# Optimization experiments

Measured on AMD Instinct MI355X. Metric: run time of the kernel, lower is better.

Reference implementation:

```python
import jax, jax.numpy as jnp
import numpy as np

H = 8        # num_heads
LN_EPS = 1e-5
NEG = -1000000.0


def setup_inputs() -> dict:
    key = jax.random.key(0)
    ks = jax.random.split(key, 8)
    B, T, D = 4, 4096, 1024
    s = 1.0 / np.sqrt(D)
    x = jax.random.normal(ks[0], (B, T, D), dtype=jnp.float32)
    tmask = (jnp.arange(T) < (3 * T) // 4).astype(jnp.float32)
    src_mask = jnp.broadcast_to(tmask[None, :, None], (B, T, 1)).astype(jnp.float32)
    Wq = jax.random.normal(ks[1], (D, D), dtype=jnp.float32) * s
    Wk = jax.random.normal(ks[2], (D, D), dtype=jnp.float32) * s
    Wv = jax.random.normal(ks[3], (D, D), dtype=jnp.float32) * s
    bq = jnp.zeros((D,), jnp.float32)
    bk = jnp.zeros((D,), jnp.float32)
    bv = jnp.zeros((D,), jnp.float32)
    gamma = jnp.ones((D,), jnp.float32)
    beta = jnp.zeros((D,), jnp.float32)
    return {"x": x, "src_mask": src_mask, "Wq": Wq, "bq": bq, "Wk": Wk,
            "bk": bk, "Wv": Wv, "bv": bv, "gamma": gamma, "beta": beta}


def reference(x, src_mask, Wq, bq, Wk, bk, Wv, bv, gamma, beta):
    B, T, D = x.shape
    Dh = D // H
    # LayerNorm (same normed input feeds q, k, v)
    mu = jnp.mean(x, axis=-1, keepdims=True)
    var = jnp.mean(jnp.square(x - mu), axis=-1, keepdims=True)
    xn = (x - mu) * jax.lax.rsqrt(var + LN_EPS) * gamma + beta
    q = xn @ Wq + bq                               # [B,T,D]
    k = xn @ Wk + bk + (1.0 - src_mask) * NEG      # mask padded timesteps
    v = (xn @ Wv + bv) * src_mask                  # zero padded values
    q = jax.nn.softmax(q.reshape(B, T, H, Dh), axis=-1)   # over feature dim
    k = jax.nn.softmax(k.reshape(B, T, H, Dh), axis=1)    # over time dim
    v = v.reshape(B, T, H, Dh)
    # efficient/linear attention: O(T * Dh^2) per head
    att = jnp.einsum('bnhd,bnhl->bhdl', k, v)      # [B,H,Dh,Dh]
    y = jnp.einsum('bnhd,bhdl->bnhl', q, att).reshape(B, T, D)
    return x + y
```

## Files before the change

kernel.cpp:

```cpp
#include <hip/hip_runtime.h>
#include <stdint.h>


typedef unsigned short u16;
typedef __attribute__((ext_vector_type(8))) short bf16x8;
typedef __attribute__((ext_vector_type(4))) float f32x4;

__device__ u16 g_WT[3][1024 * 1024];
__device__ u16 g_xn[16777216];
__device__ u16 g_ekT[16777216];
__device__ u16 g_vvT[16777216];
__device__ float g_attp[8388608];
__device__ u16 g_attT[524288];
__device__ float g_Z[4096];
__device__ int g_mflag[64];

__device__ __forceinline__ float b2f(u16 u) {
  union { unsigned int i; float f; } c;
  c.i = ((unsigned int)u) << 16;
  return c.f;
}
__device__ __forceinline__ u16 f2b(float f) {
  union { float f; unsigned int i; } c;
  c.f = f;
  unsigned int r = c.i + 0x7fffu + ((c.i >> 16) & 1u);
  return (u16)(r >> 16);
}

__device__ __forceinline__ void gload16(const void* g, void* l) {
  __builtin_amdgcn_global_load_lds(
      reinterpret_cast<const __attribute__((address_space(1))) uint32_t*>(
          reinterpret_cast<uintptr_t>(g)),
      reinterpret_cast<__attribute__((address_space(3))) uint32_t*>(
          reinterpret_cast<uintptr_t>(l)),
      16, 0, 0);
}

__device__ __forceinline__ void stage128x32(const u16* g, int stride, char* lds,
                                            int wave, int lane) {
  const int r = wave * 32 + (lane >> 2);
  const int cb = (lane & 3) * 16;
  const char* gp = (const char*)g;
  gload16(gp + (size_t)r * stride * 2 + cb, lds + wave * 2048);
  gload16(gp + (size_t)(r + 16) * stride * 2 + cb, lds + wave * 2048 + 1024);
}

__device__ __forceinline__ bf16x8 frag_ld(const char* lds, int row, int lane) {
  return *(const bf16x8*)(lds + row * 64 + ((lane >> 4) * 16));
}

__device__ __forceinline__ void tile_mfma(const char* As, const char* Bs,
                                          f32x4 (&acc)[4][4], int wm, int wn,
                                          int lane) {
  bf16x8 af[4], bfr[4];
#pragma unroll
  for (int i = 0; i < 4; i++) af[i] = frag_ld(As, wm * 64 + i * 16 + (lane & 15), lane);
#pragma unroll
  for (int j = 0; j < 4; j++) bfr[j] = frag_ld(Bs, wn * 64 + j * 16 + (lane & 15), lane);
#pragma unroll
  for (int i = 0; i < 4; i++)
#pragma unroll
    for (int j = 0; j < 4; j++)
      acc[i][j] = __builtin_amdgcn_mfma_f32_16x16x32_bf16(af[i], bfr[j], acc[i][j], 0, 0, 0);
}

__device__ __forceinline__ void stageA256(char* buf, const u16* gsrc, int h,
                                          int wave, int lane) {
#pragma unroll
  for (int i = 0; i < 2; i++) {
    const int ib = i * 64 + wave * 8;
    const int rowb = (ib & 63) | ((ib & 64) << 1) | (h << 6);
    const int row = rowb + (lane >> 3);
    const int cc = (lane & 7) ^ (row & 7);
    gload16((const char*)gsrc + ((size_t)row * 1024 + cc * 8) * 2,
            buf + rowb * 128);
  }
}
__device__ __forceinline__ void stageB256(char* buf, const u16* gsrc, int h,
                                          int wave, int lane) {
#pragma unroll
  for (int i = 0; i < 2; i++) {
    const int ib = i * 64 + wave * 8;
    const int rowb = (ib & 31) | ((ib & 96) << 1) | (h << 5);
    const int row = rowb + (lane >> 3);
    const int cc = (lane & 7) ^ (row & 7);
    gload16((const char*)gsrc + ((size_t)row * 1024 + cc * 8) * 2,
            buf + rowb * 128);
  }
}
__device__ __forceinline__ bf16x8 fragS(const char* buf, int R, int ks, int lane) {
  const int q = lane >> 4;
  return *(const bf16x8*)(buf + R * 128 + ((((ks << 2) + q) ^ (R & 7)) << 4));
}

template <bool ST>
__device__ __forceinline__ void tile_1ph(char* Ab, char* Bb, char* An, char* Bn,
                                         const u16* Agn, const u16* Bgn,
                                         f32x4 (&acc)[8][4], int wave, int lane,
                                         int wm, int wn) {
  if constexpr (ST) {
    stageA256(An, Agn, 0, wave, lane);
    stageA256(An, Agn, 1, wave, lane);
    stageB256(Bn, Bgn, 0, wave, lane);
    stageB256(Bn, Bgn, 1, wave, lane);
  }
  bf16x8 a[4][2], b[4][2];
#pragma unroll
  for (int cf = 0; cf < 4; cf++) {
    const int R = wn * 64 + cf * 16 + (lane & 15);
#pragma unroll
    for (int ks = 0; ks < 2; ks++) b[cf][ks] = fragS(Bb, R, ks, lane);
  }
#pragma unroll
  for (int rf = 0; rf < 4; rf++) {
    const int R = wm * 128 + rf * 16 + (lane & 15);
#pragma unroll
    for (int ks = 0; ks < 2; ks++) a[rf][ks] = fragS(Ab, R, ks, lane);
  }
  __builtin_amdgcn_s_setprio(1);
#pragma unroll
  for (int rf = 0; rf < 4; rf++)
#pragma unroll
    for (int cf = 0; cf < 4; cf++)
#pragma unroll
      for (int ks = 0; ks < 2; ks++)
        acc[rf][cf] = __builtin_amdgcn_mfma_f32_16x16x32_bf16(
            a[rf][ks], b[cf][ks], acc[rf][cf], 0, 0, 0);
  bf16x8 a2[4][2];
#pragma unroll
  for (int rf = 0; rf < 4; rf++) {
    const int R = wm * 128 + 64 + rf * 16 + (lane & 15);
#pragma unroll
    for (int ks = 0; ks < 2; ks++) a2[rf][ks] = fragS(Ab, R, ks, lane);
  }
#pragma unroll
  for (int rf = 0; rf < 4; rf++)
#pragma unroll
    for (int cf = 0; cf < 4; cf++)
#pragma unroll
      for (int ks = 0; ks < 2; ks++)
        acc[4 + rf][cf] = __builtin_amdgcn_mfma_f32_16x16x32_bf16(
            a2[rf][ks], b[cf][ks], acc[4 + rf][cf], 0, 0, 0);
  __builtin_amdgcn_s_setprio(0);
  if constexpr (ST) asm volatile("s_waitcnt vmcnt(0)" ::: "memory");
  __builtin_amdgcn_s_barrier();
  __builtin_amdgcn_sched_barrier(0);
}

__global__ __launch_bounds__(256) void prep_kernel(const float* __restrict__ x,
                                                   const float* __restrict__ gamma,
                                                   const float* __restrict__ beta,
                                                   const float* __restrict__ wq,
                                                   const float* __restrict__ wk,
                                                   const float* __restrict__ wv,
                                                   const float* __restrict__ mask) {
  __shared__ float ls[4], ls2[4];
  __shared__ u16 tile[32][33];
  __shared__ int sflag;
  const int bid = blockIdx.x;
  const int tid = threadIdx.x;
  if (bid < 16384) {
    if (bid < 16) g_Z[bid * 256 + tid] = 0.0f;
    if (bid < 64) {
      if (tid == 0) sflag = 0;
      __syncthreads();
      if (mask[bid * 256 + tid] > 0.5f) atomicOr(&sflag, 1);
      __syncthreads();
      if (tid == 0) g_mflag[bid] = sflag;
    }
    const int wave = tid >> 6, lane = tid & 63;
    const float* xr = x + (size_t)bid * 1024;
    float4 u = ((const float4*)xr)[tid];
    float v0 = u.x, v1 = u.y, v2 = u.z, v3 = u.w;
    float s = v0 + v1 + v2 + v3;
    float s2 = v0 * v0 + v1 * v1 + v2 * v2 + v3 * v3;
#pragma unroll
    for (int off = 32; off > 0; off >>= 1) {
      s += __shfl_down(s, off);
      s2 += __shfl_down(s2, off);
    }
    if (lane == 0) { ls[wave] = s; ls2[wave] = s2; }
    __syncthreads();
    s = ls[0] + ls[1] + ls[2] + ls[3];
    s2 = ls2[0] + ls2[1] + ls2[2] + ls2[3];
    const float mu = s * (1.0f / 1024.0f);
    const float var = fmaxf(s2 * (1.0f / 1024.0f) - mu * mu, 0.0f);
    const float rstd = rsqrtf(var + 1e-5f);
    float4 g4 = ((const float4*)gamma)[tid];
    float4 be = ((const float4*)beta)[tid];
    ushort4 o;
    o.x = f2b((v0 - mu) * rstd * g4.x + be.x);
    o.y = f2b((v1 - mu) * rstd * g4.y + be.y);
    o.z = f2b((v2 - mu) * rstd * g4.z + be.z);
    o.w = f2b((v3 - mu) * rstd * g4.w + be.w);
    *(ushort4*)(g_xn + (size_t)bid * 1024 + tid * 4) = o;
  } else {
    const int id = bid - 16384;
    const int which = id >> 10;
    const int rem = id & 1023;
    const float* src = (which == 0) ? wq : (which == 1) ? wk : wv;
    u16* dst = g_WT[which];
    const int tx = tid & 31;
    const int ty = tid >> 5;
    const int c0 = (rem & 31) * 32, r0 = (rem >> 5) * 32;
#pragma unroll
    for (int i = 0; i < 4; i++)
      tile[ty + i * 8][tx] = f2b(src[(size_t)(r0 + ty + i * 8) * 1024 + c0 + tx]);
    __syncthreads();
#pragma unroll
    for (int i = 0; i < 4; i++)
      dst[(size_t)(c0 + ty + i * 8) * 1024 + r0 + tx] = tile[tx][ty + i * 8];
  }
}

__global__ __launch_bounds__(512, 2) void gemm_kv(const float* __restrict__ bk,
                                                  const float* __restrict__ bv,
                                                  const float* __restrict__ mask) {
  __shared__ __align__(16) char smem[131072];
  const int tid = threadIdx.x, wave = tid >> 6, lane = tid & 63;
  const int L = blockIdx.x;
  const int mt = (L & 7) + 8 * (L >> 6);
  const int nt = (L >> 3) & 7;
  const int n0 = (nt & 3) * 256;
  const int z = nt >> 2;
  const int m0 = mt * 256;
  const u16* wt = z ? g_WT[2] : g_WT[1];
  const float* bias = z ? bv : bk;
  u16* outT = z ? g_vvT : g_ekT;
  const int b = m0 >> 12;
  const int t0 = m0 & 4095;
  const int wm = wave >> 2, wn = wave & 3;
  const u16* Ag = g_xn + (size_t)m0 * 1024;
  const u16* Bg = wt + (size_t)n0 * 1024;
  const size_t gbase = (size_t)b * (1024 * 4096) + (size_t)n0 * 4096 + t0;

  if (!g_mflag[m0 >> 8]) {
    const uint4 zz = {0u, 0u, 0u, 0u};
#pragma unroll
    for (int u = 0; u < 16; u++) {
      const int id = u * 512 + tid;
      const int feat = id >> 5, c = id & 31;
      *(uint4*)(outT + gbase + (size_t)feat * 4096 + c * 8) = zz;
    }
    return;
  }

  f32x4 zero = {0.f, 0.f, 0.f, 0.f};
  f32x4 acc[8][4];
#pragma unroll
  for (int i = 0; i < 8; i++)
#pragma unroll
    for (int j = 0; j < 4; j++) acc[i][j] = zero;

  stageA256(smem, Ag, 0, wave, lane);
  stageA256(smem, Ag, 1, wave, lane);
  stageB256(smem + 65536, Bg, 0, wave, lane);
  stageB256(smem + 65536, Bg, 1, wave, lane);
  asm volatile("s_waitcnt vmcnt(0)" ::: "memory");
  __builtin_amdgcn_s_barrier();

#pragma unroll 1
  for (int t = 0; t < 15; ++t) {
    const int p = t & 1;
    tile_1ph<true>(smem + p * 32768, smem + 65536 + p * 32768,
                   smem + (p ^ 1) * 32768, smem + 65536 + (p ^ 1) * 32768,
                   Ag + (t + 1) * 64, Bg + (t + 1) * 64, acc, wave, lane, wm, wn);
  }
  tile_1ph<false>(smem + 32768, smem + 65536 + 32768, smem, smem + 65536, Ag,
                  Bg, acc, wave, lane, wm, wn);

  u16* tT = (u16*)smem;
  float fsum[4] = {0.f, 0.f, 0.f, 0.f};
#pragma unroll
  for (int rf = 0; rf < 8; rf++)
#pragma unroll
    for (int r = 0; r < 4; r++) {
      const int tok = wm * 128 + rf * 16 + (lane >> 4) * 4 + r;
      const float mv = mask[m0 + tok];
#pragma unroll
      for (int cf = 0; cf < 4; cf++) {
        const int feat = wn * 64 + cf * 16 + (lane & 15);
        const float aV = acc[rf][cf][r] + bias[n0 + feat];
        float o;
        if (z)
          o = aV * mv;
        else
          o = (mv > 0.5f) ? __expf(fminf(aV, 30.0f)) : 0.0f;
        const u16 ob = f2b(o);
        tT[feat * 256 + ((((tok >> 3) ^ (feat & 7)) << 3) | (tok & 7))] = ob;
        if (!z) fsum[cf] += b2f(ob);
      }
    }
  if (!z) {
#pragma unroll
    for (int cf = 0; cf < 4; cf++) {
      float s = fsum[cf];
      s += __shfl_xor(s, 16);
      s += __shfl_xor(s, 32);
      if (lane < 16)
        atomicAdd(&g_Z[b * 1024 + n0 + wn * 64 + cf * 16 + lane], s);
    }
  }
  __syncthreads();
#pragma unroll
  for (int u = 0; u < 16; u++) {
    const int id = u * 512 + tid;
    const int feat = id >> 5, c = id & 31;
    uint4 val = *(const uint4*)&tT[feat * 256 + ((c ^ (feat & 7)) << 3)];
    *(uint4*)(outT + gbase + (size_t)feat * 4096 + c * 8) = val;
  }
}

__global__ __launch_bounds__(256) void gemm_att() {
  __shared__ __align__(16) char smem[32768];
  char* A0 = smem;
  char* B0 = smem + 8192;
  char* A1 = smem + 16384;
  char* B1 = smem + 24576;
  const int tid = threadIdx.x, wave = tid >> 6, lane = tid & 63;
  const int kc = blockIdx.x;
  const int bh = blockIdx.y;
  const int b = bh >> 3, h = bh & 7;
  if (!(g_mflag[b * 16 + kc * 2] | g_mflag[b * 16 + kc * 2 + 1])) return;
  const size_t base = (size_t)b * (1024 * 4096) + (size_t)(h * 128) * 4096;
  const int wm = wave & 1, wn = wave >> 1;
  const u16* Ag = g_ekT + base + kc * 512;
  const u16* Bg = g_vvT + base + kc * 512;

  f32x4 zero = {0.f, 0.f, 0.f, 0.f};
  f32x4 acc[4][4];
#pragma unroll
  for (int i = 0; i < 4; i++)
#pragma unroll
    for (int j = 0; j < 4; j++) acc[i][j] = zero;

  stage128x32(Ag, 4096, A0, wave, lane);
  stage128x32(Bg, 4096, B0, wave, lane);
  __syncthreads();
  for (int kt = 0; kt < 512; kt += 64) {
    stage128x32(Ag + kt + 32, 4096, A1, wave, lane);
    stage128x32(Bg + kt + 32, 4096, B1, wave, lane);
    tile_mfma(A0, B0, acc, wm, wn, lane);
    __syncthreads();
    if (kt + 64 < 512) {
      stage128x32(Ag + kt + 64, 4096, A0, wave, lane);
      stage128x32(Bg + kt + 64, 4096, B0, wave, lane);
    }
    tile_mfma(A1, B1, acc, wm, wn, lane);
    __syncthreads();
  }

  float* op = g_attp + ((size_t)(kc * 32 + bh)) * 16384;
#pragma unroll
  for (int i = 0; i < 4; i++)
#pragma unroll
    for (int r = 0; r < 4; r++) {
      const int row = wm * 64 + i * 16 + (lane >> 4) * 4 + r;
#pragma unroll
      for (int j = 0; j < 4; j++) {
        const int col = wn * 64 + j * 16 + (lane & 15);
        op[row * 128 + col] = acc[i][j][r];
      }
    }
}

__global__ __launch_bounds__(256) void attnorm_kernel() {
  const int bh = blockIdx.x;
  const int b = bh >> 3, h = bh & 7;
  const int tid = threadIdx.x;
  __shared__ float Zl[128];
  __shared__ int vfl[8];
  if (tid < 128) Zl[tid] = fmaxf(g_Z[b * 1024 + h * 128 + tid], 1e-30f);
  if (tid < 8) vfl[tid] = g_mflag[b * 16 + tid * 2] | g_mflag[b * 16 + tid * 2 + 1];
  __syncthreads();
  const int i0 = blockIdx.y * 2048;
  for (int i = i0 + tid; i < i0 + 2048; i += 256) {
    const int d = i >> 7, l = i & 127;
    float s = 0.f;
#pragma unroll
    for (int c = 0; c < 8; c++)
      if (vfl[c]) s += g_attp[((size_t)(c * 32 + bh)) * 16384 + i];
    g_attT[(size_t)bh * 16384 + l * 128 + d] = f2b(s / Zl[d]);
  }
}

__global__ __launch_bounds__(512, 2) void gemm_qy(const float* __restrict__ bq,
                                                  const float* __restrict__ x,
                                                  float* __restrict__ out) {
  __shared__ __align__(16) char smem[131072];
  __shared__ float zq4[4][256];
  const int tid = threadIdx.x, wave = tid >> 6, lane = tid & 63;
  const int L = blockIdx.x;
  const int g = L >> 3;
  const int mt = (L & 7) + 8 * (g >> 2);
  const int n0 = (g & 3) * 256;
  const int m0 = mt * 256;
  const int b = m0 >> 12;
  const int wm = wave >> 2, wn = wave & 3;
  const u16* Ag = g_xn + (size_t)m0 * 1024;
  const u16* Bg = g_WT[0] + (size_t)n0 * 1024;

  f32x4 zero = {0.f, 0.f, 0.f, 0.f};
  f32x4 acc[8][4];
#pragma unroll
  for (int i = 0; i < 8; i++)
#pragma unroll
    for (int j = 0; j < 4; j++) acc[i][j] = zero;

  stageA256(smem, Ag, 0, wave, lane);
  stageA256(smem, Ag, 1, wave, lane);
  stageB256(smem + 65536, Bg, 0, wave, lane);
  stageB256(smem + 65536, Bg, 1, wave, lane);
  asm volatile("s_waitcnt vmcnt(0)" ::: "memory");
  __builtin_amdgcn_s_barrier();

#pragma unroll 1
  for (int t = 0; t < 15; ++t) {
    const int p = t & 1;
    tile_1ph<true>(smem + p * 32768, smem + 65536 + p * 32768,
                   smem + (p ^ 1) * 32768, smem + 65536 + (p ^ 1) * 32768,
                   Ag + (t + 1) * 64, Bg + (t + 1) * 64, acc, wave, lane, wm, wn);
  }
  tile_1ph<false>(smem + 32768, smem + 65536 + 32768, smem, smem + 65536, Ag,
                  Bg, acc, wave, lane, wm, wn);

  const int hl = wn >> 1;
  const int bhh = b * 8 + (n0 >> 7) + hl;
  const u16* attb = g_attT + ((size_t)bhh << 14);
  bf16x8 bpre[4][4];
#pragma unroll
  for (int ks = 0; ks < 4; ks++)
#pragma unroll
    for (int cf = 0; cf < 4; cf++) {
      const int l = (wn & 1) * 64 + cf * 16 + (lane & 15);
      bpre[ks][cf] = *(const bf16x8*)(attb + l * 128 + ks * 32 + (lane >> 4) * 8);
    }

  u16* qs = (u16*)smem;
#pragma unroll
  for (int rf = 0; rf < 8; rf++)
#pragma unroll
    for (int r = 0; r < 4; r++) {
      const int tok = wm * 128 + rf * 16 + (lane >> 4) * 4 + r;
      float rs = 0.f;
#pragma unroll
      for (int cf = 0; cf < 4; cf++) {
        const int f = wn * 64 + cf * 16 + (lane & 15);
        const float e = __expf(fminf(acc[rf][cf][r] + bq[n0 + f], 30.0f));
        qs[tok * 256 + ((((f >> 3) ^ (tok & 31)) << 3) | (f & 7))] = f2b(e);
        rs += e;
      }
      rs += __shfl_xor(rs, 1);
      rs += __shfl_xor(rs, 2);
      rs += __shfl_xor(rs, 4);
      rs += __shfl_xor(rs, 8);
      if ((lane & 15) == 0) zq4[wn][tok] = rs;
    }
  __syncthreads();

  f32x4 acc2[8][4];
#pragma unroll
  for (int i = 0; i < 8; i++)
#pragma unroll
    for (int j = 0; j < 4; j++) acc2[i][j] = zero;

#pragma unroll
  for (int ks = 0; ks < 4; ks++) {
    bf16x8 af[8];
#pragma unroll
    for (int rf = 0; rf < 8; rf++) {
      const int tok = wm * 128 + rf * 16 + (lane & 15);
      af[rf] = *(const bf16x8*)&qs[tok * 256 +
          ((((hl << 4) + (ks << 2) + (lane >> 4)) ^ (tok & 31)) << 3)];
    }
#pragma unroll
    for (int rf = 0; rf < 8; rf++)
#pragma unroll
      for (int cf = 0; cf < 4; cf++)
        acc2[rf][cf] = __builtin_amdgcn_mfma_f32_16x16x32_bf16(
            af[rf], bpre[ks][cf], acc2[rf][cf], 0, 0, 0);
  }

#pragma unroll
  for (int rf = 0; rf < 8; rf++)
#pragma unroll
    for (int r = 0; r < 4; r++) {
      const int tok = wm * 128 + rf * 16 + (lane >> 4) * 4 + r;
      const float zq =
          fmaxf(zq4[hl * 2][tok] + zq4[hl * 2 + 1][tok], 1e-30f);
      const size_t n = (size_t)(m0 + tok);
#pragma unroll
      for (int cf = 0; cf < 4; cf++) {
        const int f = wn * 64 + cf * 16 + (lane & 15);
        const size_t idx = n * 1024 + n0 + f;
        out[idx] = x[idx] + acc2[rf][cf][r] / zq;
      }
    }
}

extern "C" void kernel_launch(void* const* d_in, const int* in_sizes, int n_in,
                              void* d_out, int out_size, void* d_ws, size_t ws_size,
                              hipStream_t stream) {
  const float* x = (const float*)d_in[0];
  const float* mask = (const float*)d_in[1];
  const float* Wq = (const float*)d_in[2];
  const float* bq = (const float*)d_in[3];
  const float* Wk = (const float*)d_in[4];
  const float* bk = (const float*)d_in[5];
  const float* Wv = (const float*)d_in[6];
  const float* bv = (const float*)d_in[7];
  const float* gamma = (const float*)d_in[8];
  const float* beta = (const float*)d_in[9];
  float* out = (float*)d_out;
  (void)d_ws; (void)ws_size;

  prep_kernel<<<dim3(16384 + 3072), 256, 0, stream>>>(x, gamma, beta, Wq, Wk, Wv, mask);
  gemm_kv<<<dim3(512), 512, 0, stream>>>(bk, bv, mask);
  gemm_att<<<dim3(8, 32), 256, 0, stream>>>();
  attnorm_kernel<<<dim3(32, 8), 256, 0, stream>>>();
  gemm_qy<<<dim3(256), 512, 0, stream>>>(bq, x, out);
}
```

Measured before the change: 339.7 us.

## Shrink gemm_kv tiles to 128x256 with K=32 stages for higher occupancy

The K/V projection GEMM moves from 256x256 output tiles with 64-wide K stages to 128x256 tiles with 32-wide K stages. This halves LDS use and accumulator registers so four blocks can share a CU, and doubles the grid to 1024 blocks. The mask flags become 128-token granular so all-padded tiles are skipped more precisely, and the downstream flag reads are updated to match. The cost is less data reuse per tile (more A/B traffic per FLOP) and twice as many barrier-synchronised K steps.

After: 350.9 us. +3.3%, slower.

```diff
diff --git a/kernel.cpp b/kernel.cpp
--- a/kernel.cpp
+++ b/kernel.cpp
@@ -13,7 +13,7 @@
 __device__ float g_attp[8388608];
 __device__ u16 g_attT[524288];
 __device__ float g_Z[4096];
-__device__ int g_mflag[64];
+__device__ int g_mflag[128];
 
 __device__ __forceinline__ float b2f(u16 u) {
   union { unsigned int i; float f; } c;
@@ -141,6 +141,57 @@
       for (int ks = 0; ks < 2; ks++)
         acc[4 + rf][cf] = __builtin_amdgcn_mfma_f32_16x16x32_bf16(
             a2[rf][ks], b[cf][ks], acc[4 + rf][cf], 0, 0, 0);
+  __builtin_amdgcn_s_setprio(0);
+  if constexpr (ST) asm volatile("s_waitcnt vmcnt(0)" ::: "memory");
+  __builtin_amdgcn_s_barrier();
+  __builtin_amdgcn_sched_barrier(0);
+}
+
+__device__ __forceinline__ void stageA128(char* buf, const u16* gsrc,
+                                          int wave, int lane) {
+  const int row = wave * 16 + (lane >> 2);
+  const int cc = (lane & 3) ^ ((row >> 1) & 3);
+  gload16((const char*)gsrc + ((size_t)row * 1024 + cc * 8) * 2,
+          buf + wave * 1024);
+}
+__device__ __forceinline__ void stageB256x32(char* buf, const u16* gsrc,
+                                             int wave, int lane) {
+#pragma unroll
+  for (int i = 0; i < 2; i++) {
+    const int row = i * 128 + wave * 16 + (lane >> 2);
+    const int cc = (lane & 3) ^ ((row >> 1) & 3);
+    gload16((const char*)gsrc + ((size_t)row * 1024 + cc * 8) * 2,
+            buf + i * 8192 + wave * 1024);
+  }
+}
+__device__ __forceinline__ bf16x8 fragS32(const char* buf, int R, int lane) {
+  const int q = lane >> 4;
+  return *(const bf16x8*)(buf + R * 64 + (((q ^ ((R >> 1) & 3))) << 4));
+}
+
+template <bool ST>
+__device__ __forceinline__ void tile32(char* Ab, char* Bb, char* An, char* Bn,
+                                       const u16* Agn, const u16* Bgn,
+                                       f32x4 (&acc)[4][4], int wave, int lane,
+                                       int wm, int wn) {
+  if constexpr (ST) {
+    stageA128(An, Agn, wave, lane);
+    stageB256x32(Bn, Bgn, wave, lane);
+  }
+  bf16x8 a[4], b[4];
+#pragma unroll
+  for (int cf = 0; cf < 4; cf++)
+    b[cf] = fragS32(Bb, wn * 64 + cf * 16 + (lane & 15), lane);
+#pragma unroll
+  for (int rf = 0; rf < 4; rf++)
+    a[rf] = fragS32(Ab, wm * 64 + rf * 16 + (lane & 15), lane);
+  __builtin_amdgcn_s_setprio(1);
+#pragma unroll
+  for (int rf = 0; rf < 4; rf++)
+#pragma unroll
+    for (int cf = 0; cf < 4; cf++)
+      acc[rf][cf] = __builtin_amdgcn_mfma_f32_16x16x32_bf16(
+          a[rf], b[cf], acc[rf][cf], 0, 0, 0);
   __builtin_amdgcn_s_setprio(0);
   if constexpr (ST) asm volatile("s_waitcnt vmcnt(0)" ::: "memory");
   __builtin_amdgcn_s_barrier();
@@ -161,10 +212,10 @@
   const int tid = threadIdx.x;
   if (bid < 16384) {
     if (bid < 16) g_Z[bid * 256 + tid] = 0.0f;
-    if (bid < 64) {
+    if (bid < 128) {
       if (tid == 0) sflag = 0;
       __syncthreads();
-      if (mask[bid * 256 + tid] > 0.5f) atomicOr(&sflag, 1);
+      if (tid < 128 && mask[bid * 128 + tid] > 0.5f) atomicOr(&sflag, 1);
       __syncthreads();
       if (tid == 0) g_mflag[bid] = sflag;
     }
@@ -213,17 +264,18 @@
   }
 }
 
-__global__ __launch_bounds__(512, 2) void gemm_kv(const float* __restrict__ bk,
+__global__ __launch_bounds__(512, 4) void gemm_kv(const float* __restrict__ bk,
                                                   const float* __restrict__ bv,
                                                   const float* __restrict__ mask) {
-  __shared__ __align__(16) char smem[131072];
+  __shared__ __align__(16) char smem[65536];
   const int tid = threadIdx.x, wave = tid >> 6, lane = tid & 63;
   const int L = blockIdx.x;
-  const int mt = (L & 7) + 8 * (L >> 6);
-  const int nt = (L >> 3) & 7;
-  const int n0 = (nt & 3) * 256;
-  const int z = nt >> 2;
-  const int m0 = mt * 256;
+  const int g = L >> 3;
+  const int mt = (L & 7) + 8 * (g >> 3);
+  const int nv = g & 7;
+  const int n0 = (nv & 3) * 256;
+  const int z = nv >> 2;
+  const int m0 = mt * 128;
   const u16* wt = z ? g_WT[2] : g_WT[1];
   const float* bias = z ? bv : bk;
   u16* outT = z ? g_vvT : g_ekT;
@@ -234,48 +286,48 @@
   const u16* Bg = wt + (size_t)n0 * 1024;
   const size_t gbase = (size_t)b * (1024 * 4096) + (size_t)n0 * 4096 + t0;
 
-  if (!g_mflag[m0 >> 8]) {
+  if (!g_mflag[m0 >> 7]) {
     const uint4 zz = {0u, 0u, 0u, 0u};
 #pragma unroll
-    for (int u = 0; u < 16; u++) {
+    for (int u = 0; u < 8; u++) {
       const int id = u * 512 + tid;
-      const int feat = id >> 5, c = id & 31;
+      const int feat = id >> 4, c = id & 15;
       *(uint4*)(outT + gbase + (size_t)feat * 4096 + c * 8) = zz;
     }
     return;
   }
 
+  char* A0 = smem;
+  char* B0 = smem + 8192;
+  char* A1 = smem + 24576;
+  char* B1 = smem + 32768;
   f32x4 zero = {0.f, 0.f, 0.f, 0.f};
-  f32x4 acc[8][4];
-#pragma unroll
-  for (int i = 0; i < 8; i++)
+  f32x4 acc[4][4];
+#pragma unroll
+  for (int i = 0; i < 4; i++)
 #pragma unroll
     for (int j = 0; j < 4; j++) acc[i][j] = zero;
 
-  stageA256(smem, Ag, 0, wave, lane);
-  stageA256(smem, Ag, 1, wave, lane);
-  stageB256(smem + 65536, Bg, 0, wave, lane);
-  stageB256(smem + 65536, Bg, 1, wave, lane);
+  stageA128(A0, Ag, wave, lane);
+  stageB256x32(B0, Bg, wave, lane);
   asm volatile("s_waitcnt vmcnt(0)" ::: "memory");
   __builtin_amdgcn_s_barrier();
 
 #pragma unroll 1
-  for (int t = 0; t < 15; ++t) {
+  for (int t = 0; t < 31; ++t) {
     const int p = t & 1;
-    tile_1ph<true>(smem + p * 32768, smem + 65536 + p * 32768,
-                   smem + (p ^ 1) * 32768, smem + 65536 + (p ^ 1) * 32768,
-                   Ag + (t + 1) * 64, Bg + (t + 1) * 64, acc, wave, lane, wm, wn);
-  }
-  tile_1ph<false>(smem + 32768, smem + 65536 + 32768, smem, smem + 65536, Ag,
-                  Bg, acc, wave, lane, wm, wn);
+    tile32<true>(p ? A1 : A0, p ? B1 : B0, p ? A0 : A1, p ? B0 : B1,
+                 Ag + (t + 1) * 32, Bg + (t + 1) * 32, acc, wave, lane, wm, wn);
+  }
+  tile32<false>(A1, B1, A0, B0, Ag, Bg, acc, wave, lane, wm, wn);
 
   u16* tT = (u16*)smem;
   float fsum[4] = {0.f, 0.f, 0.f, 0.f};
 #pragma unroll
-  for (int rf = 0; rf < 8; rf++)
+  for (int rf = 0; rf < 4; rf++)
 #pragma unroll
     for (int r = 0; r < 4; r++) {
-      const int tok = wm * 128 + rf * 16 + (lane >> 4) * 4 + r;
+      const int tok = wm * 64 + rf * 16 + (lane >> 4) * 4 + r;
       const float mv = mask[m0 + tok];
 #pragma unroll
       for (int cf = 0; cf < 4; cf++) {
@@ -287,7 +339,7 @@
         else
           o = (mv > 0.5f) ? __expf(fminf(aV, 30.0f)) : 0.0f;
         const u16 ob = f2b(o);
-        tT[feat * 256 + ((((tok >> 3) ^ (feat & 7)) << 3) | (tok & 7))] = ob;
+        tT[feat * 128 + ((((tok >> 3) ^ (feat & 15)) << 3) | (tok & 7))] = ob;
         if (!z) fsum[cf] += b2f(ob);
       }
     }
@@ -303,10 +355,10 @@
   }
   __syncthreads();
 #pragma unroll
-  for (int u = 0; u < 16; u++) {
+  for (int u = 0; u < 8; u++) {
     const int id = u * 512 + tid;
-    const int feat = id >> 5, c = id & 31;
-    uint4 val = *(const uint4*)&tT[feat * 256 + ((c ^ (feat & 7)) << 3)];
+    const int feat = id >> 4, c = id & 15;
+    uint4 val = *(const uint4*)&tT[feat * 128 + ((c ^ (feat & 15)) << 3)];
     *(uint4*)(outT + gbase + (size_t)feat * 4096 + c * 8) = val;
   }
 }
@@ -321,7 +373,9 @@
   const int kc = blockIdx.x;
   const int bh = blockIdx.y;
   const int b = bh >> 3, h = bh & 7;
-  if (!(g_mflag[b * 16 + kc * 2] | g_mflag[b * 16 + kc * 2 + 1])) return;
+  const int f0 = b * 32 + kc * 4;
+  if (!(g_mflag[f0] | g_mflag[f0 + 1] | g_mflag[f0 + 2] | g_mflag[f0 + 3]))
+    return;
   const size_t base = (size_t)b * (1024 * 4096) + (size_t)(h * 128) * 4096;
   const int wm = wave & 1, wn = wave >> 1;
   const u16* Ag = g_ekT + base + kc * 512;
@@ -371,7 +425,10 @@
   __shared__ float Zl[128];
   __shared__ int vfl[8];
   if (tid < 128) Zl[tid] = fmaxf(g_Z[b * 1024 + h * 128 + tid], 1e-30f);
-  if (tid < 8) vfl[tid] = g_mflag[b * 16 + tid * 2] | g_mflag[b * 16 + tid * 2 + 1];
+  if (tid < 8) {
+    const int f0 = b * 32 + tid * 4;
+    vfl[tid] = g_mflag[f0] | g_mflag[f0 + 1] | g_mflag[f0 + 2] | g_mflag[f0 + 3];
+  }
   __syncthreads();
   const int i0 = blockIdx.y * 2048;
   for (int i = i0 + tid; i < i0 + 2048; i += 256) {
@@ -515,7 +572,7 @@
   (void)d_ws; (void)ws_size;
 
   prep_kernel<<<dim3(16384 + 3072), 256, 0, stream>>>(x, gamma, beta, Wq, Wk, Wv, mask);
-  gemm_kv<<<dim3(512), 512, 0, stream>>>(bk, bv, mask);
+  gemm_kv<<<dim3(1024), 512, 0, stream>>>(bk, bv, mask);
   gemm_att<<<dim3(8, 32), 256, 0, stream>>>();
   attnorm_kernel<<<dim3(32, 8), 256, 0, stream>>>();
   gemm_qy<<<dim3(256), 512, 0, stream>>>(bq, x, out);
```

## Fuse K/V projection with per-tile attention partial product in one kernel

Applied to the files above, without the earlier changes.

Merges the K/V projection GEMM and the ek^T·v attention GEMM into one kernel. Each block now computes both the K and V projections for one head (128 features) over a 256-token tile, writes exp(k) and masked v to LDS, and immediately computes the 128x128 partial attention product into g_attp. This removes the round trip of the large ekT/vvT bf16 intermediates through global memory and one kernel launch. In exchange, attnorm must sum 16 partials instead of 8, and the MFMA work per block is reorganised with two accumulator sets.

Result: faster. 320.1 us (-5.8%).

```diff
diff --git a/kernel.cpp b/kernel.cpp
--- a/kernel.cpp
+++ b/kernel.cpp
@@ -8,8 +8,6 @@
 
 __device__ u16 g_WT[3][1024 * 1024];
 __device__ u16 g_xn[16777216];
-__device__ u16 g_ekT[16777216];
-__device__ u16 g_vvT[16777216];
 __device__ float g_attp[8388608];
 __device__ u16 g_attT[524288];
 __device__ float g_Z[4096];
@@ -36,34 +34,6 @@
       16, 0, 0);
 }
 
-__device__ __forceinline__ void stage128x32(const u16* g, int stride, char* lds,
-                                            int wave, int lane) {
-  const int r = wave * 32 + (lane >> 2);
-  const int cb = (lane & 3) * 16;
-  const char* gp = (const char*)g;
-  gload16(gp + (size_t)r * stride * 2 + cb, lds + wave * 2048);
-  gload16(gp + (size_t)(r + 16) * stride * 2 + cb, lds + wave * 2048 + 1024);
-}
-
-__device__ __forceinline__ bf16x8 frag_ld(const char* lds, int row, int lane) {
-  return *(const bf16x8*)(lds + row * 64 + ((lane >> 4) * 16));
-}
-
-__device__ __forceinline__ void tile_mfma(const char* As, const char* Bs,
-                                          f32x4 (&acc)[4][4], int wm, int wn,
-                                          int lane) {
-  bf16x8 af[4], bfr[4];
-#pragma unroll
-  for (int i = 0; i < 4; i++) af[i] = frag_ld(As, wm * 64 + i * 16 + (lane & 15), lane);
-#pragma unroll
-  for (int j = 0; j < 4; j++) bfr[j] = frag_ld(Bs, wn * 64 + j * 16 + (lane & 15), lane);
-#pragma unroll
-  for (int i = 0; i < 4; i++)
-#pragma unroll
-    for (int j = 0; j < 4; j++)
-      acc[i][j] = __builtin_amdgcn_mfma_f32_16x16x32_bf16(af[i], bfr[j], acc[i][j], 0, 0, 0);
-}
-
 __device__ __forceinline__ void stageA256(char* buf, const u16* gsrc, int h,
                                           int wave, int lane) {
 #pragma unroll
@@ -82,6 +52,17 @@
   for (int i = 0; i < 2; i++) {
     const int ib = i * 64 + wave * 8;
     const int rowb = (ib & 31) | ((ib & 96) << 1) | (h << 5);
+    const int row = rowb + (lane >> 3);
+    const int cc = (lane & 7) ^ (row & 7);
+    gload16((const char*)gsrc + ((size_t)row * 1024 + cc * 8) * 2,
+            buf + rowb * 128);
+  }
+}
+__device__ __forceinline__ void stageC128(char* buf, const u16* gsrc,
+                                          int wave, int lane) {
+#pragma unroll
+  for (int i = 0; i < 2; i++) {
+    const int rowb = i * 64 + wave * 8;
     const int row = rowb + (lane >> 3);
     const int cc = (lane & 7) ^ (row & 7);
     gload16((const char*)gsrc + ((size_t)row * 1024 + cc * 8) * 2,
@@ -141,6 +122,72 @@
       for (int ks = 0; ks < 2; ks++)
         acc[4 + rf][cf] = __builtin_amdgcn_mfma_f32_16x16x32_bf16(
             a2[rf][ks], b[cf][ks], acc[4 + rf][cf], 0, 0, 0);
+  __builtin_amdgcn_s_setprio(0);
+  if constexpr (ST) asm volatile("s_waitcnt vmcnt(0)" ::: "memory");
+  __builtin_amdgcn_s_barrier();
+  __builtin_amdgcn_sched_barrier(0);
+}
+
+template <bool ST>
+__device__ __forceinline__ void tile_kv(char* Ab, char* Bkb, char* Bvb,
+                                        char* An, char* Bkn, char* Bvn,
+                                        const u16* Agn, const u16* Bkgn,
+                                        const u16* Bvgn, f32x4 (&ae)[8][2],
+                                        f32x4 (&av)[8][2], int wave, int lane,
+                                        int wm, int wn) {
+  if constexpr (ST) {
+    stageA256(An, Agn, 0, wave, lane);
+    stageA256(An, Agn, 1, wave, lane);
+    stageC128(Bkn, Bkgn, wave, lane);
+    stageC128(Bvn, Bvgn, wave, lane);
+  }
+  bf16x8 bk[2][2], bv[2][2];
+#pragma unroll
+  for (int cf = 0; cf < 2; cf++) {
+    const int R = wn * 32 + cf * 16 + (lane & 15);
+#pragma unroll
+    for (int ks = 0; ks < 2; ks++) {
+      bk[cf][ks] = fragS(Bkb, R, ks, lane);
+      bv[cf][ks] = fragS(Bvb, R, ks, lane);
+    }
+  }
+  bf16x8 a[4][2];
+#pragma unroll
+  for (int rf = 0; rf < 4; rf++) {
+    const int R = wm * 128 + rf * 16 + (lane & 15);
+#pragma unroll
+    for (int ks = 0; ks < 2; ks++) a[rf][ks] = fragS(Ab, R, ks, lane);
+  }
+  __builtin_amdgcn_s_setprio(1);
+#pragma unroll
+  for (int rf = 0; rf < 4; rf++)
+#pragma unroll
+    for (int cf = 0; cf < 2; cf++)
+#pragma unroll
+      for (int ks = 0; ks < 2; ks++) {
+        ae[rf][cf] = __builtin_amdgcn_mfma_f32_16x16x32_bf16(
+            a[rf][ks], bk[cf][ks], ae[rf][cf], 0, 0, 0);
+        av[rf][cf] = __builtin_amdgcn_mfma_f32_16x16x32_bf16(
+            a[rf][ks], bv[cf][ks], av[rf][cf], 0, 0, 0);
+      }
+  bf16x8 a2[4][2];
+#pragma unroll
+  for (int rf = 0; rf < 4; rf++) {
+    const int R = wm * 128 + 64 + rf * 16 + (lane & 15);
+#pragma unroll
+    for (int ks = 0; ks < 2; ks++) a2[rf][ks] = fragS(Ab, R, ks, lane);
+  }
+#pragma unroll
+  for (int rf = 0; rf < 4; rf++)
+#pragma unroll
+    for (int cf = 0; cf < 2; cf++)
+#pragma unroll
+      for (int ks = 0; ks < 2; ks++) {
+        ae[4 + rf][cf] = __builtin_amdgcn_mfma_f32_16x16x32_bf16(
+            a2[rf][ks], bk[cf][ks], ae[4 + rf][cf], 0, 0, 0);
+        av[4 + rf][cf] = __builtin_amdgcn_mfma_f32_16x16x32_bf16(
+            a2[rf][ks], bv[cf][ks], av[4 + rf][cf], 0, 0, 0);
+      }
   __builtin_amdgcn_s_setprio(0);
   if constexpr (ST) asm volatile("s_waitcnt vmcnt(0)" ::: "memory");
   __builtin_amdgcn_s_barrier();
@@ -213,64 +260,59 @@
   }
 }
 
-__global__ __launch_bounds__(512, 2) void gemm_kv(const float* __restrict__ bk,
-                                                  const float* __restrict__ bv,
-                                                  const float* __restrict__ mask) {
+__global__ __launch_bounds__(512, 2) void gemm_kva(const float* __restrict__ bk,
+                                                   const float* __restrict__ bv,
+                                                   const float* __restrict__ mask) {
   __shared__ __align__(16) char smem[131072];
   const int tid = threadIdx.x, wave = tid >> 6, lane = tid & 63;
   const int L = blockIdx.x;
-  const int mt = (L & 7) + 8 * (L >> 6);
-  const int nt = (L >> 3) & 7;
-  const int n0 = (nt & 3) * 256;
-  const int z = nt >> 2;
-  const int m0 = mt * 256;
-  const u16* wt = z ? g_WT[2] : g_WT[1];
-  const float* bias = z ? bv : bk;
-  u16* outT = z ? g_vvT : g_ekT;
+  const int bt = L & 63;
+  const int h = L >> 6;
+  const int m0 = bt * 256;
   const int b = m0 >> 12;
-  const int t0 = m0 & 4095;
+  const int tt = bt & 15;
+  if (!g_mflag[bt]) return;
+
   const int wm = wave >> 2, wn = wave & 3;
   const u16* Ag = g_xn + (size_t)m0 * 1024;
-  const u16* Bg = wt + (size_t)n0 * 1024;
-  const size_t gbase = (size_t)b * (1024 * 4096) + (size_t)n0 * 4096 + t0;
-
-  if (!g_mflag[m0 >> 8]) {
-    const uint4 zz = {0u, 0u, 0u, 0u};
-#pragma unroll
-    for (int u = 0; u < 16; u++) {
-      const int id = u * 512 + tid;
-      const int feat = id >> 5, c = id & 31;
-      *(uint4*)(outT + gbase + (size_t)feat * 4096 + c * 8) = zz;
-    }
-    return;
-  }
+  const u16* Bkg = g_WT[1] + (size_t)(h * 128) * 1024;
+  const u16* Bvg = g_WT[2] + (size_t)(h * 128) * 1024;
+
+  char* A0 = smem;
+  char* Bk0 = smem + 32768;
+  char* Bv0 = smem + 49152;
+  char* A1 = smem + 65536;
+  char* Bk1 = smem + 98304;
+  char* Bv1 = smem + 114688;
 
   f32x4 zero = {0.f, 0.f, 0.f, 0.f};
-  f32x4 acc[8][4];
+  f32x4 ae[8][2], av[8][2];
 #pragma unroll
   for (int i = 0; i < 8; i++)
 #pragma unroll
-    for (int j = 0; j < 4; j++) acc[i][j] = zero;
-
-  stageA256(smem, Ag, 0, wave, lane);
-  stageA256(smem, Ag, 1, wave, lane);
-  stageB256(smem + 65536, Bg, 0, wave, lane);
-  stageB256(smem + 65536, Bg, 1, wave, lane);
+    for (int j = 0; j < 2; j++) { ae[i][j] = zero; av[i][j] = zero; }
+
+  stageA256(A0, Ag, 0, wave, lane);
+  stageA256(A0, Ag, 1, wave, lane);
+  stageC128(Bk0, Bkg, wave, lane);
+  stageC128(Bv0, Bvg, wave, lane);
   asm volatile("s_waitcnt vmcnt(0)" ::: "memory");
   __builtin_amdgcn_s_barrier();
 
 #pragma unroll 1
   for (int t = 0; t < 15; ++t) {
     const int p = t & 1;
-    tile_1ph<true>(smem + p * 32768, smem + 65536 + p * 32768,
-                   smem + (p ^ 1) * 32768, smem + 65536 + (p ^ 1) * 32768,
-                   Ag + (t + 1) * 64, Bg + (t + 1) * 64, acc, wave, lane, wm, wn);
-  }
-  tile_1ph<false>(smem + 32768, smem + 65536 + 32768, smem, smem + 65536, Ag,
-                  Bg, acc, wave, lane, wm, wn);
-
-  u16* tT = (u16*)smem;
-  float fsum[4] = {0.f, 0.f, 0.f, 0.f};
+    tile_kv<true>(p ? A1 : A0, p ? Bk1 : Bk0, p ? Bv1 : Bv0,
+                  p ? A0 : A1, p ? Bk0 : Bk1, p ? Bv0 : Bv1,
+                  Ag + (t + 1) * 64, Bkg + (t + 1) * 64, Bvg + (t + 1) * 64,
+                  ae, av, wave, lane, wm, wn);
+  }
+  tile_kv<false>(A1, Bk1, Bv1, A0, Bk0, Bv0, Ag, Bkg, Bvg, ae, av, wave, lane,
+                 wm, wn);
+
+  u16* ekT = (u16*)smem;
+  u16* vvT = (u16*)(smem + 65536);
+  float fsum[2] = {0.f, 0.f};
 #pragma unroll
   for (int rf = 0; rf < 8; rf++)
 #pragma unroll
@@ -278,88 +320,66 @@
       const int tok = wm * 128 + rf * 16 + (lane >> 4) * 4 + r;
       const float mv = mask[m0 + tok];
 #pragma unroll
-      for (int cf = 0; cf < 4; cf++) {
-        const int feat = wn * 64 + cf * 16 + (lane & 15);
-        const float aV = acc[rf][cf][r] + bias[n0 + feat];
-        float o;
-        if (z)
-          o = aV * mv;
-        else
-          o = (mv > 0.5f) ? __expf(fminf(aV, 30.0f)) : 0.0f;
-        const u16 ob = f2b(o);
-        tT[feat * 256 + ((((tok >> 3) ^ (feat & 7)) << 3) | (tok & 7))] = ob;
-        if (!z) fsum[cf] += b2f(ob);
+      for (int cf = 0; cf < 2; cf++) {
+        const int feat = wn * 32 + cf * 16 + (lane & 15);
+        const int slot = (((tok >> 3) ^ (feat & 31)) << 3) | (tok & 7);
+        const float ve = ae[rf][cf][r] + bk[h * 128 + feat];
+        const float oe = (mv > 0.5f) ? __expf(fminf(ve, 30.0f)) : 0.0f;
+        const u16 eb = f2b(oe);
+        ekT[feat * 256 + slot] = eb;
+        fsum[cf] += b2f(eb);
+        const float vv = (av[rf][cf][r] + bv[h * 128 + feat]) * mv;
+        vvT[feat * 256 + slot] = f2b(vv);
       }
     }
-  if (!z) {
-#pragma unroll
-    for (int cf = 0; cf < 4; cf++) {
-      float s = fsum[cf];
-      s += __shfl_xor(s, 16);
-      s += __shfl_xor(s, 32);
-      if (lane < 16)
-        atomicAdd(&g_Z[b * 1024 + n0 + wn * 64 + cf * 16 + lane], s);
-    }
+#pragma unroll
+  for (int cf = 0; cf < 2; cf++) {
+    float s = fsum[cf];
+    s += __shfl_xor(s, 16);
+    s += __shfl_xor(s, 32);
+    if (lane < 16)
+      atomicAdd(&g_Z[b * 1024 + h * 128 + wn * 32 + cf * 16 + lane], s);
   }
   __syncthreads();
-#pragma unroll
-  for (int u = 0; u < 16; u++) {
-    const int id = u * 512 + tid;
-    const int feat = id >> 5, c = id & 31;
-    uint4 val = *(const uint4*)&tT[feat * 256 + ((c ^ (feat & 7)) << 3)];
-    *(uint4*)(outT + gbase + (size_t)feat * 4096 + c * 8) = val;
-  }
-}
-
-__global__ __launch_bounds__(256) void gemm_att() {
-  __shared__ __align__(16) char smem[32768];
-  char* A0 = smem;
-  char* B0 = smem + 8192;
-  char* A1 = smem + 16384;
-  char* B1 = smem + 24576;
-  const int tid = threadIdx.x, wave = tid >> 6, lane = tid & 63;
-  const int kc = blockIdx.x;
-  const int bh = blockIdx.y;
-  const int b = bh >> 3, h = bh & 7;
-  if (!(g_mflag[b * 16 + kc * 2] | g_mflag[b * 16 + kc * 2 + 1])) return;
-  const size_t base = (size_t)b * (1024 * 4096) + (size_t)(h * 128) * 4096;
-  const int wm = wave & 1, wn = wave >> 1;
-  const u16* Ag = g_ekT + base + kc * 512;
-  const u16* Bg = g_vvT + base + kc * 512;
-
-  f32x4 zero = {0.f, 0.f, 0.f, 0.f};
-  f32x4 acc[4][4];
+
+  f32x4 acc2[4][2];
 #pragma unroll
   for (int i = 0; i < 4; i++)
 #pragma unroll
-    for (int j = 0; j < 4; j++) acc[i][j] = zero;
-
-  stage128x32(Ag, 4096, A0, wave, lane);
-  stage128x32(Bg, 4096, B0, wave, lane);
-  __syncthreads();
-  for (int kt = 0; kt < 512; kt += 64) {
-    stage128x32(Ag + kt + 32, 4096, A1, wave, lane);
-    stage128x32(Bg + kt + 32, 4096, B1, wave, lane);
-    tile_mfma(A0, B0, acc, wm, wn, lane);
-    __syncthreads();
-    if (kt + 64 < 512) {
-      stage128x32(Ag + kt + 64, 4096, A0, wave, lane);
-      stage128x32(Bg + kt + 64, 4096, B0, wave, lane);
-    }
-    tile_mfma(A1, B1, acc, wm, wn, lane);
-    __syncthreads();
-  }
-
-  float* op = g_attp + ((size_t)(kc * 32 + bh)) * 16384;
-#pragma unroll
-  for (int i = 0; i < 4; i++)
+    for (int j = 0; j < 2; j++) acc2[i][j] = zero;
+#pragma unroll
+  for (int ks = 0; ks < 8; ks++) {
+    bf16x8 aF[4], bF[2];
+#pragma unroll
+    for (int rf = 0; rf < 4; rf++) {
+      const int d = wm * 64 + rf * 16 + (lane & 15);
+      aF[rf] = *(const bf16x8*)&ekT[d * 256 +
+          ((((ks << 2) + (lane >> 4)) ^ (d & 31)) << 3)];
+    }
+#pragma unroll
+    for (int cf = 0; cf < 2; cf++) {
+      const int l = wn * 32 + cf * 16 + (lane & 15);
+      bF[cf] = *(const bf16x8*)&vvT[l * 256 +
+          ((((ks << 2) + (lane >> 4)) ^ (l & 31)) << 3)];
+    }
+#pragma unroll
+    for (int rf = 0; rf < 4; rf++)
+#pragma unroll
+      for (int cf = 0; cf < 2; cf++)
+        acc2[rf][cf] = __builtin_amdgcn_mfma_f32_16x16x32_bf16(
+            aF[rf], bF[cf], acc2[rf][cf], 0, 0, 0);
+  }
+
+  float* op = g_attp + (size_t)(tt * 32 + b * 8 + h) * 16384;
+#pragma unroll
+  for (int rf = 0; rf < 4; rf++)
 #pragma unroll
     for (int r = 0; r < 4; r++) {
-      const int row = wm * 64 + i * 16 + (lane >> 4) * 4 + r;
-#pragma unroll
-      for (int j = 0; j < 4; j++) {
-        const int col = wn * 64 + j * 16 + (lane & 15);
-        op[row * 128 + col] = acc[i][j][r];
+      const int d = wm * 64 + rf * 16 + (lane >> 4) * 4 + r;
+#pragma unroll
+      for (int cf = 0; cf < 2; cf++) {
+        const int l = wn * 32 + cf * 16 + (lane & 15);
+        op[d * 128 + l] = acc2[rf][cf][r];
       }
     }
 }
@@ -369,16 +389,16 @@
   const int b = bh >> 3, h = bh & 7;
   const int tid = threadIdx.x;
   __shared__ float Zl[128];
-  __shared__ int vfl[8];
+  __shared__ int vfl[16];
   if (tid < 128) Zl[tid] = fmaxf(g_Z[b * 1024 + h * 128 + tid], 1e-30f);
-  if (tid < 8) vfl[tid] = g_mflag[b * 16 + tid * 2] | g_mflag[b * 16 + tid * 2 + 1];
+  if (tid < 16) vfl[tid] = g_mflag[b * 16 + tid];
   __syncthreads();
   const int i0 = blockIdx.y * 2048;
   for (int i = i0 + tid; i < i0 + 2048; i += 256) {
     const int d = i >> 7, l = i & 127;
     float s = 0.f;
 #pragma unroll
-    for (int c = 0; c < 8; c++)
+    for (int c = 0; c < 16; c++)
       if (vfl[c]) s += g_attp[((size_t)(c * 32 + bh)) * 16384 + i];
     g_attT[(size_t)bh * 16384 + l * 128 + d] = f2b(s / Zl[d]);
   }
@@ -515,8 +535,7 @@
   (void)d_ws; (void)ws_size;
 
   prep_kernel<<<dim3(16384 + 3072), 256, 0, stream>>>(x, gamma, beta, Wq, Wk, Wv, mask);
-  gemm_kv<<<dim3(512), 512, 0, stream>>>(bk, bv, mask);
-  gemm_att<<<dim3(8, 32), 256, 0, stream>>>();
+  gemm_kva<<<dim3(512), 512, 0, stream>>>(bk, bv, mask);
   attnorm_kernel<<<dim3(32, 8), 256, 0, stream>>>();
   gemm_qy<<<dim3(256), 512, 0, stream>>>(bq, x, out);
 }
```
